# Kernel tuning notes

Measured on AMD Instinct MI355X. Metric: run time of the kernel, lower is better.

## Reference

```python
import jax, jax.numpy as jnp
import numpy as np

WIN = 32      # window_size
SHIFT = 16    # shift_size
EPS = 1e-5

def layernorm(x, w, b):
    mu = jnp.mean(x, axis=-1, keepdims=True)
    var = jnp.mean(jnp.square(x - mu), axis=-1, keepdims=True)
    return (x - mu) * jax.lax.rsqrt(var + EPS) * w + b

def setup_inputs() -> dict:
    key = jax.random.key(0)
    ks = jax.random.split(key, 6)
    B, N, C, H = 8, 4096, 512, 2048
    nW = N // WIN
    return {
        "q": jax.random.normal(ks[0], (B, N, C), jnp.float32),
        "kv": jax.random.normal(ks[1], (B, N, C), jnp.float32),
        "attn_mask": jax.random.normal(ks[2], (nW, WIN, WIN), jnp.float32),
        "norm1_w": jnp.ones((C,), jnp.float32),
        "norm1_b": jnp.zeros((C,), jnp.float32),
        "norm2_w": jnp.ones((C,), jnp.float32),
        "norm2_b": jnp.zeros((C,), jnp.float32),
        "fc1_w": jax.random.normal(ks[3], (H, C), jnp.float32) * 0.02,
        "fc1_b": jnp.zeros((H,), jnp.float32),
        "fc2_w": jax.random.normal(ks[4], (C, H), jnp.float32) * 0.02,
        "fc2_b": jnp.zeros((C,), jnp.float32),
    }

def reference(q, kv, attn_mask, norm1_w, norm1_b, norm2_w, norm2_b,
              fc1_w, fc1_b, fc2_w, fc2_b):
    B, N, C = q.shape
    nW = N // WIN
    shortcut = kv
    qn = layernorm(q, norm1_w, norm1_b)
    kn = layernorm(kv, norm1_w, norm1_b)
    # cyclic shift
    qs = jnp.roll(qn, -SHIFT, axis=1)
    ks = jnp.roll(kn, -SHIFT, axis=1)
    qw = qs.reshape(B * nW, WIN, C)
    kw = ks.reshape(B * nW, WIN, C)
    attn = jnp.einsum('bic,bjc->bij', qw, kw)
    attn = attn.reshape(B, nW, WIN, WIN) + attn_mask[None]
    attn = jax.nn.softmax(attn.reshape(B * nW, WIN, WIN), axis=-1)
    x = jnp.einsum('bij,bjc->bic', attn, kw)
    x = jnp.swapaxes(x, 1, 2).reshape(B * nW, WIN, C)
    # window reverse + reverse shift
    x = x.reshape(B, N, C)
    x = jnp.roll(x, SHIFT, axis=1)
    kv_out = shortcut + x
    # MLP (exact erf GELU, dropout identity at eval)
    h = layernorm(kv_out, norm2_w, norm2_b)
    h = jax.nn.gelu(h @ fc1_w.T + fc1_b, approximate=False)
    h = h @ fc2_w.T + fc2_b
    return kv_out + h
```

## Files before the change

kernel.cpp:

```cpp
#include <hip/hip_runtime.h>
#include <cstdint>
#include <cstddef>


typedef __attribute__((ext_vector_type(4))) float f32x4;
typedef __attribute__((ext_vector_type(8))) __bf16 bf16x8;
typedef __attribute__((ext_vector_type(8))) unsigned short us8;
typedef __attribute__((ext_vector_type(4))) unsigned short us4;

__device__ __forceinline__ unsigned short f2bf(float f) {
  unsigned int u = __builtin_bit_cast(unsigned int, f);
  u += 0x7fffu + ((u >> 16) & 1u);
  return (unsigned short)(u >> 16);
}

#define GLDS16(g, l)                                                         \
  __builtin_amdgcn_global_load_lds(                                          \
      (const __attribute__((address_space(1))) void*)(g),                    \
      (__attribute__((address_space(3))) void*)(l), 16, 0, 0)

__global__ __launch_bounds__(256) void wconv_kernel(
    const float* __restrict__ w1, const float* __restrict__ w2,
    unsigned short* __restrict__ o1, unsigned short* __restrict__ o2) {
  const int i = (blockIdx.x * 256 + threadIdx.x) * 4;
  const float4 a = *(const float4*)(w1 + i);
  us4 pa;
  pa[0] = f2bf(a.x); pa[1] = f2bf(a.y); pa[2] = f2bf(a.z); pa[3] = f2bf(a.w);
  *(us4*)(o1 + i) = pa;
  const float4 b = *(const float4*)(w2 + i);
  us4 pb;
  pb[0] = f2bf(b.x); pb[1] = f2bf(b.y); pb[2] = f2bf(b.z); pb[3] = f2bf(b.w);
  *(us4*)(o2 + i) = pb;
}

__global__ __launch_bounds__(256) void attn_kernel(
    const float* __restrict__ qg, const float* __restrict__ kvg,
    const float* __restrict__ maskg,
    const float* __restrict__ n1w, const float* __restrict__ n1b,
    const float* __restrict__ n2w, const float* __restrict__ n2b,
    float* __restrict__ kv_out, unsigned short* __restrict__ hn) {
  __shared__ __align__(16) float sm[2 * 32 * 516 + 32 * 36];
  float* qn = sm;
  float* kn = sm + 32 * 516;
  float* S  = sm + 2 * 32 * 516;
  float* xb = sm;

  const int t  = threadIdx.x;
  const int g  = blockIdx.x;
  const int b  = g >> 7;
  const int wi = g & 127;
  const int rg = t >> 3;
  const int lk = t & 7;

  const int n = (wi * 32 + rg + 16) & 4095;
  const float* qrow = qg  + ((size_t)b * 4096 + n) * 512;
  const float* krow = kvg + ((size_t)b * 4096 + n) * 512;

  float sq = 0.f, s2q = 0.f, sk = 0.f, s2k = 0.f;
#pragma unroll
  for (int j = 0; j < 16; ++j) {
    const int c = lk * 64 + j * 4;
    const float4 a = *(const float4*)(qrow + c);
    const float4 v = *(const float4*)(krow + c);
    *(float4*)(qn + rg * 516 + c) = a;
    *(float4*)(kn + rg * 516 + c) = v;
    sq  += a.x + a.y + a.z + a.w;
    s2q += a.x * a.x + a.y * a.y + a.z * a.z + a.w * a.w;
    sk  += v.x + v.y + v.z + v.w;
    s2k += v.x * v.x + v.y * v.y + v.z * v.z + v.w * v.w;
  }
#pragma unroll
  for (int m = 1; m < 8; m <<= 1) {
    sq += __shfl_xor(sq, m);  s2q += __shfl_xor(s2q, m);
    sk += __shfl_xor(sk, m);  s2k += __shfl_xor(s2k, m);
  }
  const float muq = sq * (1.f / 512.f);
  const float rsq = rsqrtf(s2q * (1.f / 512.f) - muq * muq + 1e-5f);
  const float muk = sk * (1.f / 512.f);
  const float rsk = rsqrtf(s2k * (1.f / 512.f) - muk * muk + 1e-5f);
#pragma unroll
  for (int j = 0; j < 16; ++j) {
    const int c = lk * 64 + j * 4;
    const float4 w4 = *(const float4*)(n1w + c);
    const float4 b4 = *(const float4*)(n1b + c);
    float4 a = *(const float4*)(qn + rg * 516 + c);
    float4 v = *(const float4*)(kn + rg * 516 + c);
    a.x = (a.x - muq) * rsq * w4.x + b4.x;
    a.y = (a.y - muq) * rsq * w4.y + b4.y;
    a.z = (a.z - muq) * rsq * w4.z + b4.z;
    a.w = (a.w - muq) * rsq * w4.w + b4.w;
    v.x = (v.x - muk) * rsk * w4.x + b4.x;
    v.y = (v.y - muk) * rsk * w4.y + b4.y;
    v.z = (v.z - muk) * rsk * w4.z + b4.z;
    v.w = (v.w - muk) * rsk * w4.w + b4.w;
    *(float4*)(qn + rg * 516 + c) = a;
    *(float4*)(kn + rg * 516 + c) = v;
  }
  __syncthreads();

  {
    float a0 = 0.f, a1 = 0.f, a2 = 0.f, a3 = 0.f;
    const float* qr = qn + rg * 516;
    const float* k0 = kn + (lk + 0)  * 516;
    const float* k1 = kn + (lk + 8)  * 516;
    const float* k2 = kn + (lk + 16) * 516;
    const float* k3 = kn + (lk + 24) * 516;
#pragma unroll 4
    for (int c = 0; c < 512; c += 4) {
      const float4 a  = *(const float4*)(qr + c);
      const float4 x0 = *(const float4*)(k0 + c);
      const float4 x1 = *(const float4*)(k1 + c);
      const float4 x2 = *(const float4*)(k2 + c);
      const float4 x3 = *(const float4*)(k3 + c);
      a0 += a.x * x0.x + a.y * x0.y + a.z * x0.z + a.w * x0.w;
      a1 += a.x * x1.x + a.y * x1.y + a.z * x1.z + a.w * x1.w;
      a2 += a.x * x2.x + a.y * x2.y + a.z * x2.z + a.w * x2.w;
      a3 += a.x * x3.x + a.y * x3.y + a.z * x3.z + a.w * x3.w;
    }
    const float* mrow = maskg + (size_t)wi * 1024 + rg * 32;
    a0 += mrow[lk];      a1 += mrow[lk + 8];
    a2 += mrow[lk + 16]; a3 += mrow[lk + 24];
    float mx = fmaxf(fmaxf(a0, a1), fmaxf(a2, a3));
#pragma unroll
    for (int m = 1; m < 8; m <<= 1) mx = fmaxf(mx, __shfl_xor(mx, m));
    const float e0 = expf(a0 - mx), e1 = expf(a1 - mx);
    const float e2 = expf(a2 - mx), e3 = expf(a3 - mx);
    float sum = e0 + e1 + e2 + e3;
#pragma unroll
    for (int m = 1; m < 8; m <<= 1) sum += __shfl_xor(sum, m);
    const float inv = 1.f / sum;
    S[rg * 36 + lk]      = e0 * inv;
    S[rg * 36 + lk + 8]  = e1 * inv;
    S[rg * 36 + lk + 16] = e2 * inv;
    S[rg * 36 + lk + 24] = e3 * inv;
  }
  __syncthreads();

  {
    float pr[32];
#pragma unroll
    for (int j4 = 0; j4 < 8; ++j4) {
      const float4 v = *(const float4*)(S + rg * 36 + j4 * 4);
      pr[j4 * 4 + 0] = v.x; pr[j4 * 4 + 1] = v.y;
      pr[j4 * 4 + 2] = v.z; pr[j4 * 4 + 3] = v.w;
    }
#pragma unroll
    for (int cc = 0; cc < 16; ++cc) {
      const int c = lk * 64 + (((cc + lk) & 15) << 2);
      float4 acc = {0.f, 0.f, 0.f, 0.f};
#pragma unroll
      for (int j = 0; j < 32; ++j) {
        const float4 kx = *(const float4*)(kn + j * 516 + c);
        acc.x += pr[j] * kx.x; acc.y += pr[j] * kx.y;
        acc.z += pr[j] * kx.z; acc.w += pr[j] * kx.w;
      }
      *(float4*)(xb + rg * 516 + c) = acc;
    }
  }
  __syncthreads();

  {
    float* orow = kv_out + ((size_t)b * 4096 + n) * 512;
    unsigned short* hrow = hn + ((size_t)b * 4096 + n) * 512;
    float4 vals[16];
    float s = 0.f, s2 = 0.f;
#pragma unroll
    for (int j = 0; j < 16; ++j) {
      const int qq = lk * 64 + j * 4;
      float4 r = *(const float4*)(krow + qq);
      const int cb = rg * 16 + (qq >> 5);
      const int ib = qq & 31;
      r.x += xb[(ib + 0) * 516 + cb];
      r.y += xb[(ib + 1) * 516 + cb];
      r.z += xb[(ib + 2) * 516 + cb];
      r.w += xb[(ib + 3) * 516 + cb];
      vals[j] = r;
      *(float4*)(orow + qq) = r;
      s  += r.x + r.y + r.z + r.w;
      s2 += r.x * r.x + r.y * r.y + r.z * r.z + r.w * r.w;
    }
#pragma unroll
    for (int m = 1; m < 8; m <<= 1) {
      s += __shfl_xor(s, m); s2 += __shfl_xor(s2, m);
    }
    const float mu   = s * (1.f / 512.f);
    const float rstd = rsqrtf(s2 * (1.f / 512.f) - mu * mu + 1e-5f);
#pragma unroll
    for (int j = 0; j < 16; ++j) {
      const int qq = lk * 64 + j * 4;
      const float4 w4 = *(const float4*)(n2w + qq);
      const float4 b4 = *(const float4*)(n2b + qq);
      const float4 r = vals[j];
      us4 h;
      h[0] = f2bf((r.x - mu) * rstd * w4.x + b4.x);
      h[1] = f2bf((r.y - mu) * rstd * w4.y + b4.y);
      h[2] = f2bf((r.z - mu) * rstd * w4.z + b4.z);
      h[3] = f2bf((r.w - mu) * rstd * w4.w + b4.w);
      *(us4*)(hrow + qq) = h;
    }
  }
}

__global__ __launch_bounds__(256) void gemm1_kernel(
    const unsigned short* __restrict__ A, const unsigned short* __restrict__ Bw,
    const float* __restrict__ bias, unsigned short* __restrict__ Y) {
  __shared__ __align__(16) char smem[32768];
  unsigned short* As = (unsigned short*)smem;
  unsigned short* Bs = (unsigned short*)(smem + 8192);

  const int tid = threadIdx.x;
  const int m0 = blockIdx.x << 7;
  const int n0 = blockIdx.y << 7;
  const int l  = tid & 63;
  const int wv = tid >> 6;
  const int wr = wv >> 1, wc = wv & 1;
  const int srow = tid >> 2;
  const int scol = (tid & 3) << 3;
  const int lrow = l & 15;
  const int lko  = (l >> 4) << 3;

  f32x4 acc[4][4] = {};

  const unsigned short* pA = A  + (size_t)(m0 + srow) * 512 + scol;
  const unsigned short* pB = Bw + (size_t)(n0 + srow) * 512 + scol;
  char* dA0 = smem + wv * 1024;
  char* dA1 = smem + 4096 + wv * 1024;
  char* dB0 = smem + 8192 + wv * 1024;
  char* dB1 = smem + 12288 + wv * 1024;

  for (int kt = 0; kt < 16; ++kt) {
    const int k0 = kt << 5;
    GLDS16(pA + k0, dA0);
    GLDS16(pA + 64 * 512 + k0, dA1);
    GLDS16(pB + k0, dB0);
    GLDS16(pB + 64 * 512 + k0, dB1);
    __syncthreads();
    bf16x8 af[4], bfr[4];
#pragma unroll
    for (int mi = 0; mi < 4; ++mi)
      af[mi] = *(const bf16x8*)(As + (wr * 64 + mi * 16 + lrow) * 32 + lko);
#pragma unroll
    for (int ni = 0; ni < 4; ++ni)
      bfr[ni] = *(const bf16x8*)(Bs + (wc * 64 + ni * 16 + lrow) * 32 + lko);
#pragma unroll
    for (int mi = 0; mi < 4; ++mi)
#pragma unroll
      for (int ni = 0; ni < 4; ++ni)
        acc[mi][ni] = __builtin_amdgcn_mfma_f32_16x16x32_bf16(
            af[mi], bfr[ni], acc[mi][ni], 0, 0, 0);
    __syncthreads();
  }

  float bn[4];
#pragma unroll
  for (int ni = 0; ni < 4; ++ni) bn[ni] = bias[n0 + wc * 64 + ni * 16 + (l & 15)];

  unsigned short* Ct = (unsigned short*)(smem + wv * 8192);
#pragma unroll
  for (int mi = 0; mi < 4; ++mi)
#pragma unroll
    for (int ni = 0; ni < 4; ++ni)
#pragma unroll
      for (int r = 0; r < 4; ++r) {
        float v = acc[mi][ni][r] + bn[ni];
        v = 0.5f * v * (1.f + erff(v * 0.70710678118654752f));
        const int row  = mi * 16 + ((l >> 4) << 2) + r;
        const int colb = (((ni * 16 + (l & 15)) << 1)) ^ ((row & 7) << 4);
        *(unsigned short*)((char*)Ct + row * 128 + colb) = f2bf(v);
      }
  __syncthreads();
#pragma unroll
  for (int it = 0; it < 8; ++it) {
    const int row = it * 8 + (l >> 3);
    const int off = ((l & 7) << 4) ^ ((row & 7) << 4);
    const us8 v = *(const us8*)((char*)Ct + row * 128 + off);
    const int grow = m0 + wr * 64 + row;
    const int gcol = n0 + wc * 64 + ((l & 7) << 3);
    *(us8*)(Y + (size_t)grow * 2048 + gcol) = v;
  }
}

__global__ __launch_bounds__(256) void gemm2_kernel(
    const unsigned short* __restrict__ A, const unsigned short* __restrict__ Bw,
    const float* __restrict__ bias, const float* __restrict__ res,
    float* __restrict__ out) {
  __shared__ __align__(16) char smem[65536];
  unsigned short* As = (unsigned short*)smem;
  unsigned short* Bs = (unsigned short*)(smem + 8192);

  const int tid = threadIdx.x;
  const int m0 = blockIdx.x << 7;
  const int n0 = blockIdx.y << 7;
  const int l  = tid & 63;
  const int wv = tid >> 6;
  const int wr = wv >> 1, wc = wv & 1;
  const int srow = tid >> 2;
  const int scol = (tid & 3) << 3;
  const int lrow = l & 15;
  const int lko  = (l >> 4) << 3;

  f32x4 acc[4][4] = {};

  const unsigned short* pA = A  + (size_t)(m0 + srow) * 2048 + scol;
  const unsigned short* pB = Bw + (size_t)(n0 + srow) * 2048 + scol;
  char* dA0 = smem + wv * 1024;
  char* dA1 = smem + 4096 + wv * 1024;
  char* dB0 = smem + 8192 + wv * 1024;
  char* dB1 = smem + 12288 + wv * 1024;

  for (int kt = 0; kt < 64; ++kt) {
    const int k0 = kt << 5;
    GLDS16(pA + k0, dA0);
    GLDS16(pA + 64 * 2048 + k0, dA1);
    GLDS16(pB + k0, dB0);
    GLDS16(pB + 64 * 2048 + k0, dB1);
    __syncthreads();
    bf16x8 af[4], bfr[4];
#pragma unroll
    for (int mi = 0; mi < 4; ++mi)
      af[mi] = *(const bf16x8*)(As + (wr * 64 + mi * 16 + lrow) * 32 + lko);
#pragma unroll
    for (int ni = 0; ni < 4; ++ni)
      bfr[ni] = *(const bf16x8*)(Bs + (wc * 64 + ni * 16 + lrow) * 32 + lko);
#pragma unroll
    for (int mi = 0; mi < 4; ++mi)
#pragma unroll
      for (int ni = 0; ni < 4; ++ni)
        acc[mi][ni] = __builtin_amdgcn_mfma_f32_16x16x32_bf16(
            af[mi], bfr[ni], acc[mi][ni], 0, 0, 0);
    __syncthreads();
  }

  float* Ct = (float*)(smem + wv * 16384);
#pragma unroll
  for (int mi = 0; mi < 4; ++mi)
#pragma unroll
    for (int ni = 0; ni < 4; ++ni)
#pragma unroll
      for (int r = 0; r < 4; ++r) {
        const int row  = mi * 16 + ((l >> 4) << 2) + r;
        const int col  = ni * 16 + (l & 15);
        const int colb = (col << 2) ^ ((row & 7) << 4);
        *(float*)((char*)Ct + (row << 8) + colb) = acc[mi][ni][r];
      }
  __syncthreads();
#pragma unroll
  for (int it = 0; it < 16; ++it) {
    const int row = it * 4 + (l >> 4);
    const int off = ((l & 15) << 4) ^ ((row & 7) << 4);
    f32x4 v = *(const f32x4*)((char*)Ct + (row << 8) + off);
    const int grow = m0 + wr * 64 + row;
    const int gcol = n0 + wc * 64 + ((l & 15) << 2);
    const f32x4 b4 = *(const f32x4*)(bias + gcol);
    const f32x4 r4 = *(const f32x4*)(res + (size_t)grow * 512 + gcol);
    v = v + b4 + r4;
    *(f32x4*)(out + (size_t)grow * 512 + gcol) = v;
  }
}

extern "C" void kernel_launch(void* const* d_in, const int* in_sizes, int n_in,
                              void* d_out, int out_size, void* d_ws,
                              size_t ws_size, hipStream_t stream) {
  const float* q   = (const float*)d_in[0];
  const float* kv  = (const float*)d_in[1];
  const float* msk = (const float*)d_in[2];
  const float* n1w = (const float*)d_in[3];
  const float* n1b = (const float*)d_in[4];
  const float* n2w = (const float*)d_in[5];
  const float* n2b = (const float*)d_in[6];
  const float* w1  = (const float*)d_in[7];
  const float* b1  = (const float*)d_in[8];
  const float* w2  = (const float*)d_in[9];
  const float* b2  = (const float*)d_in[10];
  float* out = (float*)d_out;

  char* ws = (char*)d_ws;
  float*          kv_out = (float*)ws;
  unsigned short* hn     = (unsigned short*)(ws + 67108864);
  unsigned short* Y1     = (unsigned short*)(ws + 100663296);
  unsigned short* w1b    = (unsigned short*)(ws + 234881024);
  unsigned short* w2b    = (unsigned short*)(ws + 236978176);

  hipLaunchKernelGGL(wconv_kernel, dim3(1024), dim3(256), 0, stream,
                     w1, w2, w1b, w2b);
  hipLaunchKernelGGL(attn_kernel, dim3(1024), dim3(256), 0, stream,
                     q, kv, msk, n1w, n1b, n2w, n2b, kv_out, hn);
  hipLaunchKernelGGL(gemm1_kernel, dim3(256, 16), dim3(256), 0, stream,
                     hn, w1b, b1, Y1);
  hipLaunchKernelGGL(gemm2_kernel, dim3(256, 4), dim3(256), 0, stream,
                     Y1, w2b, b2, kv_out, out);
}
```

Measured before the change: 600.6 us.

## Move window attention to bf16 MFMA with split stats kernel and double-buffer GEMMs

Replaces the scalar-FMA window attention with MFMA-based QK^T, using a hi/lo bf16 split to keep near-fp32 accuracy. Per-row layernorm statistics now come from a separate stats kernel. The P·K product folds the layernorm algebraically into per-column scale and bias terms and reads raw kv from global memory. Both GEMMs now double-buffer their LDS tiles, and gemm2 writes its epilogue directly instead of staging through shared memory. The trade-offs are an extra kernel launch, re-reading q/kv from global, strided scalar kv loads, and bf16 rounding of P·V.

```diff
diff --git a/kernel.cpp b/kernel.cpp
--- a/kernel.cpp
+++ b/kernel.cpp
@@ -3,10 +3,11 @@
 #include <cstddef>
 
 
-typedef __attribute__((ext_vector_type(4))) float f32x4;
-typedef __attribute__((ext_vector_type(8))) __bf16 bf16x8;
-typedef __attribute__((ext_vector_type(8))) unsigned short us8;
-typedef __attribute__((ext_vector_type(4))) unsigned short us4;
+typedef __attribute__((ext_vector_type(4)))  float f32x4;
+typedef __attribute__((ext_vector_type(16))) float f32x16;
+typedef __attribute__((ext_vector_type(8)))  __bf16 bf16x8;
+typedef __attribute__((ext_vector_type(8)))  unsigned short us8;
+typedef __attribute__((ext_vector_type(4)))  unsigned short us4;
 
 __device__ __forceinline__ unsigned short f2bf(float f) {
   unsigned int u = __builtin_bit_cast(unsigned int, f);
@@ -23,180 +24,216 @@
     const float* __restrict__ w1, const float* __restrict__ w2,
     unsigned short* __restrict__ o1, unsigned short* __restrict__ o2) {
   const int i = (blockIdx.x * 256 + threadIdx.x) * 4;
-  const float4 a = *(const float4*)(w1 + i);
-  us4 pa;
-  pa[0] = f2bf(a.x); pa[1] = f2bf(a.y); pa[2] = f2bf(a.z); pa[3] = f2bf(a.w);
+  const f32x4 a = *(const f32x4*)(w1 + i);
+  us4 pa; pa[0]=f2bf(a[0]); pa[1]=f2bf(a[1]); pa[2]=f2bf(a[2]); pa[3]=f2bf(a[3]);
   *(us4*)(o1 + i) = pa;
-  const float4 b = *(const float4*)(w2 + i);
-  us4 pb;
-  pb[0] = f2bf(b.x); pb[1] = f2bf(b.y); pb[2] = f2bf(b.z); pb[3] = f2bf(b.w);
+  const f32x4 b = *(const f32x4*)(w2 + i);
+  us4 pb; pb[0]=f2bf(b[0]); pb[1]=f2bf(b[1]); pb[2]=f2bf(b[2]); pb[3]=f2bf(b[3]);
   *(us4*)(o2 + i) = pb;
 }
 
-__global__ __launch_bounds__(256) void attn_kernel(
+__global__ __launch_bounds__(256) void stats_kernel(
+    const float* __restrict__ qg, const float* __restrict__ kvg,
+    float* __restrict__ stats) {
+  const int gw = (blockIdx.x * 256 + threadIdx.x) >> 6;
+  const int l  = threadIdx.x & 63;
+  const int s  = gw & 1;
+  const int row = gw >> 1;
+  const float* src = (s ? kvg : qg) + (size_t)row * 512 + l * 8;
+  const f32x4 v0 = *(const f32x4*)(src);
+  const f32x4 v1 = *(const f32x4*)(src + 4);
+  float a = 0.f, a2 = 0.f;
+#pragma unroll
+  for (int m = 0; m < 4; ++m) {
+    a += v0[m] + v1[m];
+    a2 += v0[m] * v0[m] + v1[m] * v1[m];
+  }
+#pragma unroll
+  for (int mm = 1; mm <= 32; mm <<= 1) {
+    a += __shfl_xor(a, mm); a2 += __shfl_xor(a2, mm);
+  }
+  if (l == 0) {
+    const float mu = a * (1.f / 512.f);
+    const float rs = rsqrtf(a2 * (1.f / 512.f) - mu * mu + 1e-5f);
+    *(float2*)(stats + (size_t)row * 4 + s * 2) = make_float2(mu, rs);
+  }
+}
+
+__global__ __launch_bounds__(128) void attn2_kernel(
     const float* __restrict__ qg, const float* __restrict__ kvg,
     const float* __restrict__ maskg,
     const float* __restrict__ n1w, const float* __restrict__ n1b,
     const float* __restrict__ n2w, const float* __restrict__ n2b,
+    const float* __restrict__ stats,
     float* __restrict__ kv_out, unsigned short* __restrict__ hn) {
-  __shared__ __align__(16) float sm[2 * 32 * 516 + 32 * 36];
-  float* qn = sm;
-  float* kn = sm + 32 * 516;
-  float* S  = sm + 2 * 32 * 516;
-  float* xb = sm;
+  __shared__ __align__(16) float xch[2][4][64][4];
 
   const int t  = threadIdx.x;
+  const int h  = t >> 6;
+  const int l  = t & 63;
+  const int il = l & 31;
+  const int hi = l >> 5;
   const int g  = blockIdx.x;
   const int b  = g >> 7;
   const int wi = g & 127;
-  const int rg = t >> 3;
-  const int lk = t & 7;
-
-  const int n = (wi * 32 + rg + 16) & 4095;
-  const float* qrow = qg  + ((size_t)b * 4096 + n) * 512;
-  const float* krow = kvg + ((size_t)b * 4096 + n) * 512;
-
-  float sq = 0.f, s2q = 0.f, sk = 0.f, s2k = 0.f;
-#pragma unroll
-  for (int j = 0; j < 16; ++j) {
-    const int c = lk * 64 + j * 4;
-    const float4 a = *(const float4*)(qrow + c);
-    const float4 v = *(const float4*)(krow + c);
-    *(float4*)(qn + rg * 516 + c) = a;
-    *(float4*)(kn + rg * 516 + c) = v;
-    sq  += a.x + a.y + a.z + a.w;
-    s2q += a.x * a.x + a.y * a.y + a.z * a.z + a.w * a.w;
-    sk  += v.x + v.y + v.z + v.w;
-    s2k += v.x * v.x + v.y * v.y + v.z * v.z + v.w * v.w;
-  }
-#pragma unroll
-  for (int m = 1; m < 8; m <<= 1) {
-    sq += __shfl_xor(sq, m);  s2q += __shfl_xor(s2q, m);
-    sk += __shfl_xor(sk, m);  s2k += __shfl_xor(s2k, m);
-  }
-  const float muq = sq * (1.f / 512.f);
-  const float rsq = rsqrtf(s2q * (1.f / 512.f) - muq * muq + 1e-5f);
-  const float muk = sk * (1.f / 512.f);
-  const float rsk = rsqrtf(s2k * (1.f / 512.f) - muk * muk + 1e-5f);
-#pragma unroll
-  for (int j = 0; j < 16; ++j) {
-    const int c = lk * 64 + j * 4;
-    const float4 w4 = *(const float4*)(n1w + c);
-    const float4 b4 = *(const float4*)(n1b + c);
-    float4 a = *(const float4*)(qn + rg * 516 + c);
-    float4 v = *(const float4*)(kn + rg * 516 + c);
-    a.x = (a.x - muq) * rsq * w4.x + b4.x;
-    a.y = (a.y - muq) * rsq * w4.y + b4.y;
-    a.z = (a.z - muq) * rsq * w4.z + b4.z;
-    a.w = (a.w - muq) * rsq * w4.w + b4.w;
-    v.x = (v.x - muk) * rsk * w4.x + b4.x;
-    v.y = (v.y - muk) * rsk * w4.y + b4.y;
-    v.z = (v.z - muk) * rsk * w4.z + b4.z;
-    v.w = (v.w - muk) * rsk * w4.w + b4.w;
-    *(float4*)(qn + rg * 516 + c) = a;
-    *(float4*)(kn + rg * 516 + c) = v;
+  const int wbase = wi * 32 + 16;
+
+  const int nrow = (wbase + il) & 4095;
+  const size_t rowidx = (size_t)b * 4096 + nrow;
+  const float* qrow = qg  + rowidx * 512;
+  const float* krow = kvg + rowidx * 512;
+  const f32x4 st = *(const f32x4*)(stats + rowidx * 4);
+
+  f32x16 sacc = {};
+#pragma unroll
+  for (int t16 = 0; t16 < 16; ++t16) {
+    const int kk = h * 256 + t16 * 16 + hi * 8;
+    const f32x4 qa = *(const f32x4*)(qrow + kk);
+    const f32x4 qb = *(const f32x4*)(qrow + kk + 4);
+    const f32x4 ka = *(const f32x4*)(krow + kk);
+    const f32x4 kb = *(const f32x4*)(krow + kk + 4);
+    const f32x4 wa = *(const f32x4*)(n1w + kk);
+    const f32x4 wb = *(const f32x4*)(n1w + kk + 4);
+    const f32x4 ba = *(const f32x4*)(n1b + kk);
+    const f32x4 bb = *(const f32x4*)(n1b + kk + 4);
+    bf16x8 qh, ql, kh, kl;
+#pragma unroll
+    for (int e = 0; e < 8; ++e) {
+      const float qe = (e < 4) ? qa[e] : qb[e - 4];
+      const float ke = (e < 4) ? ka[e] : kb[e - 4];
+      const float we = (e < 4) ? wa[e] : wb[e - 4];
+      const float be = (e < 4) ? ba[e] : bb[e - 4];
+      const float qn = (qe - st[0]) * st[1] * we + be;
+      const float kn = (ke - st[2]) * st[3] * we + be;
+      const __bf16 qhb = (__bf16)qn;
+      const __bf16 khb = (__bf16)kn;
+      qh[e] = qhb; ql[e] = (__bf16)(qn - (float)qhb);
+      kh[e] = khb; kl[e] = (__bf16)(kn - (float)khb);
+    }
+    sacc = __builtin_amdgcn_mfma_f32_32x32x16_bf16(kh, qh, sacc, 0, 0, 0);
+    sacc = __builtin_amdgcn_mfma_f32_32x32x16_bf16(kh, ql, sacc, 0, 0, 0);
+    sacc = __builtin_amdgcn_mfma_f32_32x32x16_bf16(kl, qh, sacc, 0, 0, 0);
+  }
+
+#pragma unroll
+  for (int qd = 0; qd < 4; ++qd) {
+    f32x4 v = {sacc[qd*4+0], sacc[qd*4+1], sacc[qd*4+2], sacc[qd*4+3]};
+    *(f32x4*)&xch[h][qd][l][0] = v;
   }
   __syncthreads();
-
-  {
-    float a0 = 0.f, a1 = 0.f, a2 = 0.f, a3 = 0.f;
-    const float* qr = qn + rg * 516;
-    const float* k0 = kn + (lk + 0)  * 516;
-    const float* k1 = kn + (lk + 8)  * 516;
-    const float* k2 = kn + (lk + 16) * 516;
-    const float* k3 = kn + (lk + 24) * 516;
-#pragma unroll 4
-    for (int c = 0; c < 512; c += 4) {
-      const float4 a  = *(const float4*)(qr + c);
-      const float4 x0 = *(const float4*)(k0 + c);
-      const float4 x1 = *(const float4*)(k1 + c);
-      const float4 x2 = *(const float4*)(k2 + c);
-      const float4 x3 = *(const float4*)(k3 + c);
-      a0 += a.x * x0.x + a.y * x0.y + a.z * x0.z + a.w * x0.w;
-      a1 += a.x * x1.x + a.y * x1.y + a.z * x1.z + a.w * x1.w;
-      a2 += a.x * x2.x + a.y * x2.y + a.z * x2.z + a.w * x2.w;
-      a3 += a.x * x3.x + a.y * x3.y + a.z * x3.z + a.w * x3.w;
-    }
-    const float* mrow = maskg + (size_t)wi * 1024 + rg * 32;
-    a0 += mrow[lk];      a1 += mrow[lk + 8];
-    a2 += mrow[lk + 16]; a3 += mrow[lk + 24];
-    float mx = fmaxf(fmaxf(a0, a1), fmaxf(a2, a3));
-#pragma unroll
-    for (int m = 1; m < 8; m <<= 1) mx = fmaxf(mx, __shfl_xor(mx, m));
-    const float e0 = expf(a0 - mx), e1 = expf(a1 - mx);
-    const float e2 = expf(a2 - mx), e3 = expf(a3 - mx);
-    float sum = e0 + e1 + e2 + e3;
-#pragma unroll
-    for (int m = 1; m < 8; m <<= 1) sum += __shfl_xor(sum, m);
-    const float inv = 1.f / sum;
-    S[rg * 36 + lk]      = e0 * inv;
-    S[rg * 36 + lk + 8]  = e1 * inv;
-    S[rg * 36 + lk + 16] = e2 * inv;
-    S[rg * 36 + lk + 24] = e3 * inv;
-  }
-  __syncthreads();
-
-  {
-    float pr[32];
-#pragma unroll
-    for (int j4 = 0; j4 < 8; ++j4) {
-      const float4 v = *(const float4*)(S + rg * 36 + j4 * 4);
-      pr[j4 * 4 + 0] = v.x; pr[j4 * 4 + 1] = v.y;
-      pr[j4 * 4 + 2] = v.z; pr[j4 * 4 + 3] = v.w;
-    }
-#pragma unroll
-    for (int cc = 0; cc < 16; ++cc) {
-      const int c = lk * 64 + (((cc + lk) & 15) << 2);
-      float4 acc = {0.f, 0.f, 0.f, 0.f};
-#pragma unroll
-      for (int j = 0; j < 32; ++j) {
-        const float4 kx = *(const float4*)(kn + j * 516 + c);
-        acc.x += pr[j] * kx.x; acc.y += pr[j] * kx.y;
-        acc.z += pr[j] * kx.z; acc.w += pr[j] * kx.w;
+  float sv[16];
+#pragma unroll
+  for (int qd = 0; qd < 4; ++qd) {
+    const f32x4 v = *(const f32x4*)&xch[1 - h][qd][l][0];
+#pragma unroll
+    for (int m = 0; m < 4; ++m) sv[qd*4+m] = sacc[qd*4+m] + v[m];
+  }
+
+  const float* mrow = maskg + (size_t)wi * 1024 + il * 32;
+  float mx = -1e30f;
+#pragma unroll
+  for (int r = 0; r < 16; ++r) {
+    const int j = (r & 3) + 8 * (r >> 2) + 4 * hi;
+    sv[r] += mrow[j];
+    mx = fmaxf(mx, sv[r]);
+  }
+  mx = fmaxf(mx, __shfl_xor(mx, 32));
+  float P[16], sum = 0.f;
+#pragma unroll
+  for (int r = 0; r < 16; ++r) { P[r] = __expf(sv[r] - mx); sum += P[r]; }
+  sum += __shfl_xor(sum, 32);
+  const float inv = 1.f / sum;
+
+  const float rs_own = st[3];
+  const float ms_own = st[2] * st[3];
+  float Pp[16], beta = 0.f;
+#pragma unroll
+  for (int r = 0; r < 16; ++r) {
+    const int j = (r & 3) + 8 * (r >> 2) + 4 * hi;
+    const float rsj = __shfl(rs_own, j);
+    const float msj = __shfl(ms_own, j);
+    P[r] *= inv;
+    beta -= P[r] * msj;
+    Pp[r] = P[r] * rsj;
+  }
+  beta += __shfl_xor(beta, 32);
+  float breg[16];
+#pragma unroll
+  for (int r = 0; r < 16; ++r) {
+    const int ir = (r & 3) + 8 * (r >> 2) + 4 * hi;
+    breg[r] = __shfl(beta, ir);
+  }
+
+  float Ps[16];
+#pragma unroll
+  for (int r = 0; r < 16; ++r) Ps[r] = __shfl_xor(Pp[r], 32);
+  bf16x8 pa[2];
+#pragma unroll
+  for (int s = 0; s < 2; ++s) {
+#pragma unroll
+    for (int m = 0; m < 8; ++m) {
+      float v;
+      if (m < 4) v = (hi == 0) ? Pp[8*s+m] : Ps[8*s+m+4];
+      else       v = (hi == 1) ? Pp[8*s+m] : Ps[8*s+m-4];
+      pa[s][m] = (__bf16)v;
+    }
+  }
+
+  const size_t bbase = (size_t)b * 4096;
+#pragma unroll 2
+  for (int nt = 0; nt < 8; ++nt) {
+    const int c = h * 256 + nt * 32 + il;
+    const float* kvc = kvg + bbase * 512 + c;
+    bf16x8 pb0, pb1;
+#pragma unroll
+    for (int e = 0; e < 8; ++e) {
+      const int j0 = 8 * hi + e;
+      const int r0 = (wbase + j0) & 4095;
+      pb0[e] = (__bf16)kvc[(size_t)r0 * 512];
+      const int r1 = (wbase + j0 + 16) & 4095;
+      pb1[e] = (__bf16)kvc[(size_t)r1 * 512];
+    }
+    f32x16 x = {};
+    x = __builtin_amdgcn_mfma_f32_32x32x16_bf16(pa[0], pb0, x, 0, 0, 0);
+    x = __builtin_amdgcn_mfma_f32_32x32x16_bf16(pa[1], pb1, x, 0, 0, 0);
+
+    const int p  = h * 16 + nt * 2 + (il >> 4);
+    const int np = (wbase + p) & 4095;
+    const size_t orow = (bbase + np) * 512;
+    const float w1c = n1w[c], b1c = n1b[c];
+    float ov[16], s1 = 0.f, s2 = 0.f;
+#pragma unroll
+    for (int qd = 0; qd < 4; ++qd) {
+      const int q0 = (il & 15) * 32 + 8 * qd + 4 * hi;
+      const f32x4 rv = *(const f32x4*)(kvg + orow + q0);
+      f32x4 o;
+#pragma unroll
+      for (int m = 0; m < 4; ++m) {
+        const int r = qd * 4 + m;
+        const float xv = w1c * (x[r] + breg[r]) + b1c;
+        o[m] = xv + rv[m];
+        s1 += o[m]; s2 += o[m] * o[m];
+        ov[r] = o[m];
       }
-      *(float4*)(xb + rg * 516 + c) = acc;
-    }
-  }
-  __syncthreads();
-
-  {
-    float* orow = kv_out + ((size_t)b * 4096 + n) * 512;
-    unsigned short* hrow = hn + ((size_t)b * 4096 + n) * 512;
-    float4 vals[16];
-    float s = 0.f, s2 = 0.f;
-#pragma unroll
-    for (int j = 0; j < 16; ++j) {
-      const int qq = lk * 64 + j * 4;
-      float4 r = *(const float4*)(krow + qq);
-      const int cb = rg * 16 + (qq >> 5);
-      const int ib = qq & 31;
-      r.x += xb[(ib + 0) * 516 + cb];
-      r.y += xb[(ib + 1) * 516 + cb];
-      r.z += xb[(ib + 2) * 516 + cb];
-      r.w += xb[(ib + 3) * 516 + cb];
-      vals[j] = r;
-      *(float4*)(orow + qq) = r;
-      s  += r.x + r.y + r.z + r.w;
-      s2 += r.x * r.x + r.y * r.y + r.z * r.z + r.w * r.w;
-    }
-#pragma unroll
-    for (int m = 1; m < 8; m <<= 1) {
-      s += __shfl_xor(s, m); s2 += __shfl_xor(s2, m);
-    }
-    const float mu   = s * (1.f / 512.f);
-    const float rstd = rsqrtf(s2 * (1.f / 512.f) - mu * mu + 1e-5f);
-#pragma unroll
-    for (int j = 0; j < 16; ++j) {
-      const int qq = lk * 64 + j * 4;
-      const float4 w4 = *(const float4*)(n2w + qq);
-      const float4 b4 = *(const float4*)(n2b + qq);
-      const float4 r = vals[j];
-      us4 h;
-      h[0] = f2bf((r.x - mu) * rstd * w4.x + b4.x);
-      h[1] = f2bf((r.y - mu) * rstd * w4.y + b4.y);
-      h[2] = f2bf((r.z - mu) * rstd * w4.z + b4.z);
-      h[3] = f2bf((r.w - mu) * rstd * w4.w + b4.w);
-      *(us4*)(hrow + qq) = h;
+      *(f32x4*)(kv_out + orow + q0) = o;
+    }
+#pragma unroll
+    for (int mm = 1; mm <= 8; mm <<= 1) {
+      s1 += __shfl_xor(s1, mm); s2 += __shfl_xor(s2, mm);
+    }
+    s1 += __shfl_xor(s1, 32); s2 += __shfl_xor(s2, 32);
+    const float mu2 = s1 * (1.f / 512.f);
+    const float rr  = rsqrtf(s2 * (1.f / 512.f) - mu2 * mu2 + 1e-5f);
+#pragma unroll
+    for (int qd = 0; qd < 4; ++qd) {
+      const int q0 = (il & 15) * 32 + 8 * qd + 4 * hi;
+      const f32x4 w2v = *(const f32x4*)(n2w + q0);
+      const f32x4 b2v = *(const f32x4*)(n2b + q0);
+      us4 hh;
+#pragma unroll
+      for (int m = 0; m < 4; ++m)
+        hh[m] = f2bf((ov[qd*4+m] - mu2) * rr * w2v[m] + b2v[m]);
+      *(us4*)(hn + orow + q0) = hh;
     }
   }
 }
@@ -205,8 +242,6 @@
     const unsigned short* __restrict__ A, const unsigned short* __restrict__ Bw,
     const float* __restrict__ bias, unsigned short* __restrict__ Y) {
   __shared__ __align__(16) char smem[32768];
-  unsigned short* As = (unsigned short*)smem;
-  unsigned short* Bs = (unsigned short*)(smem + 8192);
 
   const int tid = threadIdx.x;
   const int m0 = blockIdx.x << 7;
@@ -220,21 +255,25 @@
   const int lko  = (l >> 4) << 3;
 
   f32x4 acc[4][4] = {};
-
   const unsigned short* pA = A  + (size_t)(m0 + srow) * 512 + scol;
   const unsigned short* pB = Bw + (size_t)(n0 + srow) * 512 + scol;
-  char* dA0 = smem + wv * 1024;
-  char* dA1 = smem + 4096 + wv * 1024;
-  char* dB0 = smem + 8192 + wv * 1024;
-  char* dB1 = smem + 12288 + wv * 1024;
-
+
+#define G1_STAGE(p, kt)                                                      \
+  {                                                                          \
+    char* base = smem + (p) * 16384;                                         \
+    GLDS16(pA + (kt) * 32,            base + wv * 1024);                     \
+    GLDS16(pA + 64 * 512 + (kt) * 32, base + 4096 + wv * 1024);              \
+    GLDS16(pB + (kt) * 32,            base + 8192 + wv * 1024);              \
+    GLDS16(pB + 64 * 512 + (kt) * 32, base + 12288 + wv * 1024);             \
+  }
+
+  G1_STAGE(0, 0);
+  __syncthreads();
   for (int kt = 0; kt < 16; ++kt) {
-    const int k0 = kt << 5;
-    GLDS16(pA + k0, dA0);
-    GLDS16(pA + 64 * 512 + k0, dA1);
-    GLDS16(pB + k0, dB0);
-    GLDS16(pB + 64 * 512 + k0, dB1);
-    __syncthreads();
+    const int p = kt & 1;
+    if (kt < 15) G1_STAGE(p ^ 1, kt + 1);
+    const unsigned short* As = (const unsigned short*)(smem + p * 16384);
+    const unsigned short* Bs = As + 4096;
     bf16x8 af[4], bfr[4];
 #pragma unroll
     for (int mi = 0; mi < 4; ++mi)
@@ -284,9 +323,7 @@
     const unsigned short* __restrict__ A, const unsigned short* __restrict__ Bw,
     const float* __restrict__ bias, const float* __restrict__ res,
     float* __restrict__ out) {
-  __shared__ __align__(16) char smem[65536];
-  unsigned short* As = (unsigned short*)smem;
-  unsigned short* Bs = (unsigned short*)(smem + 8192);
+  __shared__ __align__(16) char smem[32768];
 
   const int tid = threadIdx.x;
   const int m0 = blockIdx.x << 7;
@@ -300,21 +337,25 @@
   const int lko  = (l >> 4) << 3;
 
   f32x4 acc[4][4] = {};
-
   const unsigned short* pA = A  + (size_t)(m0 + srow) * 2048 + scol;
   const unsigned short* pB = Bw + (size_t)(n0 + srow) * 2048 + scol;
-  char* dA0 = smem + wv * 1024;
-  char* dA1 = smem + 4096 + wv * 1024;
-  char* dB0 = smem + 8192 + wv * 1024;
-  char* dB1 = smem + 12288 + wv * 1024;
-
+
+#define G2_STAGE(p, kt)                                                      \
+  {                                                                          \
+    char* base = smem + (p) * 16384;                                         \
+    GLDS16(pA + (kt) * 32,             base + wv * 1024);                    \
+    GLDS16(pA + 64 * 2048 + (kt) * 32, base + 4096 + wv * 1024);             \
+    GLDS16(pB + (kt) * 32,             base + 8192 + wv * 1024);             \
+    GLDS16(pB + 64 * 2048 + (kt) * 32, base + 12288 + wv * 1024);            \
+  }
+
+  G2_STAGE(0, 0);
+  __syncthreads();
   for (int kt = 0; kt < 64; ++kt) {
-    const int k0 = kt << 5;
-    GLDS16(pA + k0, dA0);
-    GLDS16(pA + 64 * 2048 + k0, dA1);
-    GLDS16(pB + k0, dB0);
-    GLDS16(pB + 64 * 2048 + k0, dB1);
-    __syncthreads();
+    const int p = kt & 1;
+    if (kt < 63) G2_STAGE(p ^ 1, kt + 1);
+    const unsigned short* As = (const unsigned short*)(smem + p * 16384);
+    const unsigned short* Bs = As + 4096;
     bf16x8 af[4], bfr[4];
 #pragma unroll
     for (int mi = 0; mi < 4; ++mi)
@@ -331,30 +372,18 @@
     __syncthreads();
   }
 
-  float* Ct = (float*)(smem + wv * 16384);
-#pragma unroll
-  for (int mi = 0; mi < 4; ++mi)
-#pragma unroll
-    for (int ni = 0; ni < 4; ++ni)
+#pragma unroll
+  for (int ni = 0; ni < 4; ++ni) {
+    const int col = n0 + wc * 64 + ni * 16 + (l & 15);
+    const float bb = bias[col];
+#pragma unroll
+    for (int mi = 0; mi < 4; ++mi)
 #pragma unroll
       for (int r = 0; r < 4; ++r) {
-        const int row  = mi * 16 + ((l >> 4) << 2) + r;
-        const int col  = ni * 16 + (l & 15);
-        const int colb = (col << 2) ^ ((row & 7) << 4);
-        *(float*)((char*)Ct + (row << 8) + colb) = acc[mi][ni][r];
+        const int row = m0 + wr * 64 + mi * 16 + ((l >> 4) << 2) + r;
+        const size_t idx = (size_t)row * 512 + col;
+        out[idx] = acc[mi][ni][r] + bb + res[idx];
       }
-  __syncthreads();
-#pragma unroll
-  for (int it = 0; it < 16; ++it) {
-    const int row = it * 4 + (l >> 4);
-    const int off = ((l & 15) << 4) ^ ((row & 7) << 4);
-    f32x4 v = *(const f32x4*)((char*)Ct + (row << 8) + off);
-    const int grow = m0 + wr * 64 + row;
-    const int gcol = n0 + wc * 64 + ((l & 15) << 2);
-    const f32x4 b4 = *(const f32x4*)(bias + gcol);
-    const f32x4 r4 = *(const f32x4*)(res + (size_t)grow * 512 + gcol);
-    v = v + b4 + r4;
-    *(f32x4*)(out + (size_t)grow * 512 + gcol) = v;
   }
 }
 
@@ -380,11 +409,14 @@
   unsigned short* Y1     = (unsigned short*)(ws + 100663296);
   unsigned short* w1b    = (unsigned short*)(ws + 234881024);
   unsigned short* w2b    = (unsigned short*)(ws + 236978176);
+  float*          stats  = (float*)(ws + 239075328);
 
   hipLaunchKernelGGL(wconv_kernel, dim3(1024), dim3(256), 0, stream,
                      w1, w2, w1b, w2b);
-  hipLaunchKernelGGL(attn_kernel, dim3(1024), dim3(256), 0, stream,
-                     q, kv, msk, n1w, n1b, n2w, n2b, kv_out, hn);
+  hipLaunchKernelGGL(stats_kernel, dim3(16384), dim3(256), 0, stream,
+                     q, kv, stats);
+  hipLaunchKernelGGL(attn2_kernel, dim3(1024), dim3(128), 0, stream,
+                     q, kv, msk, n1w, n1b, n2w, n2b, stats, kv_out, hn);
   hipLaunchKernelGGL(gemm1_kernel, dim3(256, 16), dim3(256), 0, stream,
                      hn, w1b, b1, Y1);
   hipLaunchKernelGGL(gemm2_kernel, dim3(256, 4), dim3(256), 0, stream,
```

Measured after the change: 509.6 us. 15.2% less time.
